# Optimization experiments

Hardware: AMD Instinct MI355X
Metric: run time of the kernel (lower is better)

## Reference

```python
import jax, jax.numpy as jnp
import numpy as np

OUT_FEATURES = 11008
IN_FEATURES = 4096
PACKED_LEN = OUT_FEATURES * IN_FEATURES // 4  # 4 ternary vals per byte, 2 bits each


def setup_inputs() -> dict:
    key = jax.random.key(0)
    k1, k2, k3 = jax.random.split(key, 3)
    x = jax.random.normal(k1, (4, 1024, IN_FEATURES), dtype=jnp.float32)
    packed_weight = jax.random.randint(k2, (PACKED_LEN,), 0, 256, dtype=jnp.int32)
    weight_scale = jax.random.uniform(k3, (1,), dtype=jnp.float32)
    return {"x": x, "packed_weight": packed_weight, "weight_scale": weight_scale}


def _dequantize_weight(packed_weight, weight_scale):
    shifts = jnp.arange(0, 8, 2, dtype=jnp.int32)          # [4]
    q = ((packed_weight[:, None] >> shifts) & 3) - 1        # [P, 4]
    q = q.reshape(OUT_FEATURES, IN_FEATURES).astype(jnp.float32)
    return q * weight_scale.reshape(())                      # dequantize


def reference(x, packed_weight, weight_scale):
    w = _dequantize_weight(packed_weight, weight_scale)      # [out, in]
    # F.linear: y = x @ w.T  (bias=False)
    return jnp.einsum('bsi,oi->bso', x, w)
```

## Files before the change

### kernel.cpp

```cpp
#include <hip/hip_runtime.h>
#include <hip/hip_bf16.h>

#define OUT_F 11008
#define IN_F  4096
#define M_DIM 4096

typedef __attribute__((ext_vector_type(8))) short bf16x8;
typedef __attribute__((ext_vector_type(4))) float f32x4;
typedef __attribute__((ext_vector_type(8))) unsigned short us8;

__device__ __forceinline__ unsigned short f2bf_rne(float f) {
    unsigned u = __builtin_bit_cast(unsigned, f);
    u += 0x7fffu + ((u >> 16) & 1u);
    return (unsigned short)(u >> 16);
}

__global__ void cvt_x_kernel(const float* __restrict__ x,
                             unsigned short* __restrict__ xb) {
    size_t i = ((size_t)blockIdx.x * blockDim.x + threadIdx.x) * 8;
    float4 a = *(const float4*)(x + i);
    float4 b = *(const float4*)(x + i + 4);
    us8 o;
    o[0] = f2bf_rne(a.x); o[1] = f2bf_rne(a.y);
    o[2] = f2bf_rne(a.z); o[3] = f2bf_rne(a.w);
    o[4] = f2bf_rne(b.x); o[5] = f2bf_rne(b.y);
    o[6] = f2bf_rne(b.z); o[7] = f2bf_rne(b.w);
    *(us8*)(xb + i) = o;
}

__global__ void unpack_w_kernel(const int* __restrict__ pw,
                                unsigned short* __restrict__ wb) {
    size_t i = (size_t)blockIdx.x * blockDim.x + threadIdx.x;
    int4 v = ((const int4*)pw)[i];
    const unsigned long long LUT = 0x40003F800000BF80ull;
    us8 o0, o1;
#pragma unroll
    for (int j = 0; j < 4; j++) {
        o0[j]     = (unsigned short)(LUT >> (((v.x >> (2 * j)) & 3) * 16));
        o0[4 + j] = (unsigned short)(LUT >> (((v.y >> (2 * j)) & 3) * 16));
        o1[j]     = (unsigned short)(LUT >> (((v.z >> (2 * j)) & 3) * 16));
        o1[4 + j] = (unsigned short)(LUT >> (((v.w >> (2 * j)) & 3) * 16));
    }
    ((us8*)wb)[i * 2]     = o0;
    ((us8*)wb)[i * 2 + 1] = o1;
}

#define LGKM0() do { asm volatile("s_waitcnt lgkmcnt(0)" ::: "memory"); \
                     __builtin_amdgcn_sched_barrier(0); } while (0)
#define VMCNT(n) do { asm volatile("s_waitcnt vmcnt(" #n ")" ::: "memory"); \
                      __builtin_amdgcn_sched_barrier(0); } while (0)

__global__ __launch_bounds__(512, 2) void gemm_kernel(
    const unsigned short* __restrict__ A,
    const unsigned short* __restrict__ B,
    float* __restrict__ C,
    const float* __restrict__ scale_ptr) {
    constexpr int K  = IN_F;
    constexpr int N  = OUT_F;
    constexpr int NT = K / 64;

    __shared__ unsigned short lds[2][2][2][256][32];

    const int tid  = threadIdx.x;
    const int wave = tid >> 6;
    const int lane = tid & 63;
    const int quad = lane >> 4;
    const int mrow = lane & 15;
    const int sw   = quad ^ ((mrow >> 1) & 3);

    const int srow = lane >> 2;
    const int sseg = (lane & 3) ^ ((lane >> 3) & 3);

    const int lin = blockIdx.x;
    const int xcd = lin & 7;
    const int q   = lin >> 3;
    const int bm  = xcd * 2 + q / 43;
    const int bn  = q % 43;

    const int wm = (wave >> 2) * 128;
    const int wn = (wave & 3) * 64;

    const unsigned short* Ag = A + (size_t)bm * 256 * K;
    const unsigned short* Bg = B + (size_t)bn * 256 * K;

    f32x4 acc[8][4];
#pragma unroll
    for (int i = 0; i < 8; i++)
#pragma unroll
        for (int j = 0; j < 4; j++) acc[i][j] = (f32x4){0.f, 0.f, 0.f, 0.f};

    auto STAGE = [&](int mat, int nb, int h, int kbase) {
#pragma unroll
        for (int c = 0; c < 2; ++c) {
            const int chunk = wave * 2 + c;
            const int grow  = chunk * 16 + srow;
            const unsigned short* src =
                (mat ? Bg : Ag) + (size_t)grow * K + kbase + sseg * 8;
            __builtin_amdgcn_global_load_lds(
                (const __attribute__((address_space(1))) void*)src,
                (__attribute__((address_space(3))) void*)
                    (&lds[nb][mat][h][0][0] + chunk * 512),
                16, 0, 0);
        }
    };

    STAGE(0, 0, 0, 0);
    STAGE(1, 0, 0, 0);
    STAGE(0, 0, 1, 32);
    STAGE(1, 0, 1, 32);
    VMCNT(4);
    __builtin_amdgcn_s_barrier();

    bf16x8 a[8], b0, b1, b2, b3;

#pragma unroll 2
    for (int kt = 0; kt < NT; ++kt) {
        const int  buf  = kt & 1;
        const int  nbuf = buf ^ 1;
        const bool pf   = (kt + 1 < NT);
        const int  kn   = (kt + 1) * 64;

#pragma unroll
        for (int t = 0; t < 8; ++t)
            a[t] = *(const bf16x8*)&lds[buf][0][0][wm + t * 16 + mrow][sw * 8];
        b0 = *(const bf16x8*)&lds[buf][1][0][wn +  0 + mrow][sw * 8];
        b1 = *(const bf16x8*)&lds[buf][1][0][wn + 16 + mrow][sw * 8];
        if (pf) STAGE(0, nbuf, 0, kn);
        __builtin_amdgcn_s_barrier();
        LGKM0();
        __builtin_amdgcn_s_setprio(1);
#pragma unroll
        for (int t = 0; t < 8; ++t) {
            acc[t][0] = __builtin_amdgcn_mfma_f32_16x16x32_bf16(a[t], b0, acc[t][0], 0, 0, 0);
            acc[t][1] = __builtin_amdgcn_mfma_f32_16x16x32_bf16(a[t], b1, acc[t][1], 0, 0, 0);
        }
        __builtin_amdgcn_s_setprio(0);
        __builtin_amdgcn_s_barrier();

        b2 = *(const bf16x8*)&lds[buf][1][0][wn + 32 + mrow][sw * 8];
        b3 = *(const bf16x8*)&lds[buf][1][0][wn + 48 + mrow][sw * 8];
        if (pf) STAGE(1, nbuf, 0, kn);
        __builtin_amdgcn_s_barrier();
        LGKM0();
        __builtin_amdgcn_s_setprio(1);
#pragma unroll
        for (int t = 0; t < 8; ++t) {
            acc[t][2] = __builtin_amdgcn_mfma_f32_16x16x32_bf16(a[t], b2, acc[t][2], 0, 0, 0);
            acc[t][3] = __builtin_amdgcn_mfma_f32_16x16x32_bf16(a[t], b3, acc[t][3], 0, 0, 0);
        }
        __builtin_amdgcn_s_setprio(0);
        if (pf) { VMCNT(4); } else { VMCNT(0); }
        __builtin_amdgcn_s_barrier();

#pragma unroll
        for (int t = 0; t < 8; ++t)
            a[t] = *(const bf16x8*)&lds[buf][0][1][wm + t * 16 + mrow][sw * 8];
        b0 = *(const bf16x8*)&lds[buf][1][1][wn +  0 + mrow][sw * 8];
        b1 = *(const bf16x8*)&lds[buf][1][1][wn + 16 + mrow][sw * 8];
        if (pf) STAGE(0, nbuf, 1, kn + 32);
        __builtin_amdgcn_s_barrier();
        LGKM0();
        __builtin_amdgcn_s_setprio(1);
#pragma unroll
        for (int t = 0; t < 8; ++t) {
            acc[t][0] = __builtin_amdgcn_mfma_f32_16x16x32_bf16(a[t], b0, acc[t][0], 0, 0, 0);
            acc[t][1] = __builtin_amdgcn_mfma_f32_16x16x32_bf16(a[t], b1, acc[t][1], 0, 0, 0);
        }
        __builtin_amdgcn_s_setprio(0);
        __builtin_amdgcn_s_barrier();

        b2 = *(const bf16x8*)&lds[buf][1][1][wn + 32 + mrow][sw * 8];
        b3 = *(const bf16x8*)&lds[buf][1][1][wn + 48 + mrow][sw * 8];
        if (pf) STAGE(1, nbuf, 1, kn + 32);
        __builtin_amdgcn_s_barrier();
        LGKM0();
        __builtin_amdgcn_s_setprio(1);
#pragma unroll
        for (int t = 0; t < 8; ++t) {
            acc[t][2] = __builtin_amdgcn_mfma_f32_16x16x32_bf16(a[t], b2, acc[t][2], 0, 0, 0);
            acc[t][3] = __builtin_amdgcn_mfma_f32_16x16x32_bf16(a[t], b3, acc[t][3], 0, 0, 0);
        }
        __builtin_amdgcn_s_setprio(0);
        if (pf) { VMCNT(4); }
        __builtin_amdgcn_s_barrier();
    }

    const float scale = *scale_ptr;
    float* Cg = C + (size_t)(bm * 256 + wm) * N + bn * 256 + wn;
#pragma unroll
    for (int i = 0; i < 8; ++i) {
#pragma unroll
        for (int j = 0; j < 4; ++j) {
#pragma unroll
            for (int r = 0; r < 4; ++r) {
                const int row = i * 16 + quad * 4 + r;
                const int col = j * 16 + mrow;
                Cg[(size_t)row * N + col] = acc[i][j][r] * scale;
            }
        }
    }
}

extern "C" void kernel_launch(void* const* d_in, const int* in_sizes, int n_in,
                              void* d_out, int out_size, void* d_ws, size_t ws_size,
                              hipStream_t stream) {
    const float* x   = (const float*)d_in[0];
    const int* pw    = (const int*)d_in[1];
    const float* wsc = (const float*)d_in[2];

    float* out = (float*)d_out;

    unsigned short* xb = (unsigned short*)d_ws;
    unsigned short* wb = (unsigned short*)((char*)d_ws + (size_t)M_DIM * IN_F * 2);

    cvt_x_kernel<<<8192, 256, 0, stream>>>(x, xb);

    unpack_w_kernel<<<11008, 256, 0, stream>>>(pw, wb);

    gemm_kernel<<<688, 512, 0, stream>>>(xb, wb, out, wsc);
}
```

Baseline: 587.6 us.

## Merge prep kernels and replace hand-interleaved GEMM pipeline with simple double buffering

Merges the x conversion and weight unpack kernels into one launch that dispatches on block index, saving one kernel launch. The GEMM main loop drops the hand-scheduled interleaving of LDS reads, partial global prefetches, priority hints and explicit waitcnt/barriers. It now issues all four prefetch stages up front, computes both K halves with a full 8x4 MFMA block each, and ends every iteration with one __syncthreads. This simplifies the code but gives up the fine-grained overlap of memory and compute, and leaves scheduling to the compiler.

```diff
diff --git a/kernel.cpp b/kernel.cpp
--- a/kernel.cpp
+++ b/kernel.cpp
@@ -15,40 +15,36 @@
     return (unsigned short)(u >> 16);
 }
 
-__global__ void cvt_x_kernel(const float* __restrict__ x,
-                             unsigned short* __restrict__ xb) {
-    size_t i = ((size_t)blockIdx.x * blockDim.x + threadIdx.x) * 8;
-    float4 a = *(const float4*)(x + i);
-    float4 b = *(const float4*)(x + i + 4);
-    us8 o;
-    o[0] = f2bf_rne(a.x); o[1] = f2bf_rne(a.y);
-    o[2] = f2bf_rne(a.z); o[3] = f2bf_rne(a.w);
-    o[4] = f2bf_rne(b.x); o[5] = f2bf_rne(b.y);
-    o[6] = f2bf_rne(b.z); o[7] = f2bf_rne(b.w);
-    *(us8*)(xb + i) = o;
+__global__ void prep_kernel(const float* __restrict__ x,
+                            unsigned short* __restrict__ xb,
+                            const int* __restrict__ pw,
+                            unsigned short* __restrict__ wb) {
+    if (blockIdx.x < 8192) {
+        size_t i = ((size_t)blockIdx.x * blockDim.x + threadIdx.x) * 8;
+        float4 a = *(const float4*)(x + i);
+        float4 b = *(const float4*)(x + i + 4);
+        us8 o;
+        o[0] = f2bf_rne(a.x); o[1] = f2bf_rne(a.y);
+        o[2] = f2bf_rne(a.z); o[3] = f2bf_rne(a.w);
+        o[4] = f2bf_rne(b.x); o[5] = f2bf_rne(b.y);
+        o[6] = f2bf_rne(b.z); o[7] = f2bf_rne(b.w);
+        *(us8*)(xb + i) = o;
+    } else {
+        size_t i = ((size_t)(blockIdx.x - 8192)) * blockDim.x + threadIdx.x;
+        int4 v = ((const int4*)pw)[i];
+        const unsigned long long LUT = 0x40003F800000BF80ull;
+        us8 o0, o1;
+#pragma unroll
+        for (int j = 0; j < 4; j++) {
+            o0[j]     = (unsigned short)(LUT >> (((v.x >> (2 * j)) & 3) * 16));
+            o0[4 + j] = (unsigned short)(LUT >> (((v.y >> (2 * j)) & 3) * 16));
+            o1[j]     = (unsigned short)(LUT >> (((v.z >> (2 * j)) & 3) * 16));
+            o1[4 + j] = (unsigned short)(LUT >> (((v.w >> (2 * j)) & 3) * 16));
+        }
+        ((us8*)wb)[i * 2]     = o0;
+        ((us8*)wb)[i * 2 + 1] = o1;
+    }
 }
-
-__global__ void unpack_w_kernel(const int* __restrict__ pw,
-                                unsigned short* __restrict__ wb) {
-    size_t i = (size_t)blockIdx.x * blockDim.x + threadIdx.x;
-    int4 v = ((const int4*)pw)[i];
-    const unsigned long long LUT = 0x40003F800000BF80ull;
-    us8 o0, o1;
-#pragma unroll
-    for (int j = 0; j < 4; j++) {
-        o0[j]     = (unsigned short)(LUT >> (((v.x >> (2 * j)) & 3) * 16));
-        o0[4 + j] = (unsigned short)(LUT >> (((v.y >> (2 * j)) & 3) * 16));
-        o1[j]     = (unsigned short)(LUT >> (((v.z >> (2 * j)) & 3) * 16));
-        o1[4 + j] = (unsigned short)(LUT >> (((v.w >> (2 * j)) & 3) * 16));
-    }
-    ((us8*)wb)[i * 2]     = o0;
-    ((us8*)wb)[i * 2 + 1] = o1;
-}
-
-#define LGKM0() do { asm volatile("s_waitcnt lgkmcnt(0)" ::: "memory"); \
-                     __builtin_amdgcn_sched_barrier(0); } while (0)
-#define VMCNT(n) do { asm volatile("s_waitcnt vmcnt(" #n ")" ::: "memory"); \
-                      __builtin_amdgcn_sched_barrier(0); } while (0)
 
 __global__ __launch_bounds__(512, 2) void gemm_kernel(
     const unsigned short* __restrict__ A,
@@ -108,81 +104,39 @@
     STAGE(1, 0, 0, 0);
     STAGE(0, 0, 1, 32);
     STAGE(1, 0, 1, 32);
-    VMCNT(4);
-    __builtin_amdgcn_s_barrier();
+    __syncthreads();
 
-    bf16x8 a[8], b0, b1, b2, b3;
-
-#pragma unroll 2
     for (int kt = 0; kt < NT; ++kt) {
         const int  buf  = kt & 1;
         const int  nbuf = buf ^ 1;
         const bool pf   = (kt + 1 < NT);
         const int  kn   = (kt + 1) * 64;
 
-#pragma unroll
-        for (int t = 0; t < 8; ++t)
-            a[t] = *(const bf16x8*)&lds[buf][0][0][wm + t * 16 + mrow][sw * 8];
-        b0 = *(const bf16x8*)&lds[buf][1][0][wn +  0 + mrow][sw * 8];
-        b1 = *(const bf16x8*)&lds[buf][1][0][wn + 16 + mrow][sw * 8];
-        if (pf) STAGE(0, nbuf, 0, kn);
-        __builtin_amdgcn_s_barrier();
-        LGKM0();
-        __builtin_amdgcn_s_setprio(1);
-#pragma unroll
-        for (int t = 0; t < 8; ++t) {
-            acc[t][0] = __builtin_amdgcn_mfma_f32_16x16x32_bf16(a[t], b0, acc[t][0], 0, 0, 0);
-            acc[t][1] = __builtin_amdgcn_mfma_f32_16x16x32_bf16(a[t], b1, acc[t][1], 0, 0, 0);
+        if (pf) {
+            STAGE(0, nbuf, 0, kn);
+            STAGE(1, nbuf, 0, kn);
+            STAGE(0, nbuf, 1, kn + 32);
+            STAGE(1, nbuf, 1, kn + 32);
         }
-        __builtin_amdgcn_s_setprio(0);
-        __builtin_amdgcn_s_barrier();
-
-        b2 = *(const bf16x8*)&lds[buf][1][0][wn + 32 + mrow][sw * 8];
-        b3 = *(const bf16x8*)&lds[buf][1][0][wn + 48 + mrow][sw * 8];
-        if (pf) STAGE(1, nbuf, 0, kn);
-        __builtin_amdgcn_s_barrier();
-        LGKM0();
-        __builtin_amdgcn_s_setprio(1);
-#pragma unroll
-        for (int t = 0; t < 8; ++t) {
-            acc[t][2] = __builtin_amdgcn_mfma_f32_16x16x32_bf16(a[t], b2, acc[t][2], 0, 0, 0);
-            acc[t][3] = __builtin_amdgcn_mfma_f32_16x16x32_bf16(a[t], b3, acc[t][3], 0, 0, 0);
-        }
-        __builtin_amdgcn_s_setprio(0);
-        if (pf) { VMCNT(4); } else { VMCNT(0); }
-        __builtin_amdgcn_s_barrier();
 
 #pragma unroll
-        for (int t = 0; t < 8; ++t)
-            a[t] = *(const bf16x8*)&lds[buf][0][1][wm + t * 16 + mrow][sw * 8];
-        b0 = *(const bf16x8*)&lds[buf][1][1][wn +  0 + mrow][sw * 8];
-        b1 = *(const bf16x8*)&lds[buf][1][1][wn + 16 + mrow][sw * 8];
-        if (pf) STAGE(0, nbuf, 1, kn + 32);
-        __builtin_amdgcn_s_barrier();
-        LGKM0();
-        __builtin_amdgcn_s_setprio(1);
+        for (int h = 0; h < 2; ++h) {
+            bf16x8 a[8], b[4];
 #pragma unroll
-        for (int t = 0; t < 8; ++t) {
-            acc[t][0] = __builtin_amdgcn_mfma_f32_16x16x32_bf16(a[t], b0, acc[t][0], 0, 0, 0);
-            acc[t][1] = __builtin_amdgcn_mfma_f32_16x16x32_bf16(a[t], b1, acc[t][1], 0, 0, 0);
+            for (int t = 0; t < 8; ++t)
+                a[t] = *(const bf16x8*)&lds[buf][0][h][wm + t * 16 + mrow][sw * 8];
+#pragma unroll
+            for (int j = 0; j < 4; ++j)
+                b[j] = *(const bf16x8*)&lds[buf][1][h][wn + j * 16 + mrow][sw * 8];
+#pragma unroll
+            for (int t = 0; t < 8; ++t)
+#pragma unroll
+                for (int j = 0; j < 4; ++j)
+                    acc[t][j] = __builtin_amdgcn_mfma_f32_16x16x32_bf16(
+                        a[t], b[j], acc[t][j], 0, 0, 0);
         }
-        __builtin_amdgcn_s_setprio(0);
-        __builtin_amdgcn_s_barrier();
 
-        b2 = *(const bf16x8*)&lds[buf][1][1][wn + 32 + mrow][sw * 8];
-        b3 = *(const bf16x8*)&lds[buf][1][1][wn + 48 + mrow][sw * 8];
-        if (pf) STAGE(1, nbuf, 1, kn + 32);
-        __builtin_amdgcn_s_barrier();
-        LGKM0();
-        __builtin_amdgcn_s_setprio(1);
-#pragma unroll
-        for (int t = 0; t < 8; ++t) {
-            acc[t][2] = __builtin_amdgcn_mfma_f32_16x16x32_bf16(a[t], b2, acc[t][2], 0, 0, 0);
-            acc[t][3] = __builtin_amdgcn_mfma_f32_16x16x32_bf16(a[t], b3, acc[t][3], 0, 0, 0);
-        }
-        __builtin_amdgcn_s_setprio(0);
-        if (pf) { VMCNT(4); }
-        __builtin_amdgcn_s_barrier();
+        __syncthreads();
     }
 
     const float scale = *scale_ptr;
@@ -213,9 +167,7 @@
     unsigned short* xb = (unsigned short*)d_ws;
     unsigned short* wb = (unsigned short*)((char*)d_ws + (size_t)M_DIM * IN_F * 2);
 
-    cvt_x_kernel<<<8192, 256, 0, stream>>>(x, xb);
-
-    unpack_w_kernel<<<11008, 256, 0, stream>>>(pw, wb);
+    prep_kernel<<<8192 + 11008, 256, 0, stream>>>(x, xb, pw, wb);
 
     gemm_kernel<<<688, 512, 0, stream>>>(xb, wb, out, wsc);
 }
```

Result: slower. 603.0 us (+2.6%).
